# Kernel optimization log

Measured on AMD Instinct MI355X. Metric: run time of the kernel, lower is better.

The kernel has to match this reference:

```python
import jax, jax.numpy as jnp
import numpy as np

_SCAN_CHUNK = 32


def _causal_decay_scan(x, decay, init):
    """Inclusive scan out[t] = decay*out[t-1] + x[t], chunked closed form.
    x: [B,H,T,D], decay: [1,H,1], init: [B,H,D]. Returns [B,H,T,D]."""
    B, H, T, D = x.shape
    C = min(_SCAN_CHUNK, T)
    assert T % C == 0
    nC = T // C
    log_decay = jnp.log(jnp.clip(decay.astype(jnp.float32), 1e-8, None))  # [1,H,1]
    c_idx = jnp.arange(C, dtype=jnp.float32)
    log_p = log_decay[..., None] * c_idx.reshape(1, 1, C, 1)              # [1,H,C,1]
    p = jnp.exp(log_p)
    inv_p = jnp.exp(-log_p)
    init_p = jnp.exp(log_decay[..., None] * (c_idx + 1.0).reshape(1, 1, C, 1))
    # [nC, B, H, C, D] so lax.scan chains chunk states causally
    xc = x.reshape(B, H, nC, C, D).transpose(2, 0, 1, 3, 4).astype(jnp.float32)

    def step(state, chunk):  # state [B,H,D], chunk [B,H,C,D]
        cs = jnp.cumsum(chunk * inv_p, axis=2)
        out = cs * p + state[:, :, None, :] * init_p
        return out[:, :, -1, :], out

    _, outs = jax.lax.scan(step, init.astype(jnp.float32), xc)
    return outs.transpose(1, 2, 0, 3, 4).reshape(B, H, T, D).astype(x.dtype)


def _phi(x):
    return jax.nn.elu(x) + 1.0


def setup_inputs() -> dict:
    key = jax.random.key(0)
    ks = jax.random.split(key, 5)
    B, T, hidden, H = 4, 4096, 1024, 16
    s = 1.0 / np.sqrt(hidden)
    x = jax.random.normal(ks[0], (B, T, hidden), dtype=jnp.float32)
    Wqkv = jax.random.normal(ks[1], (3 * hidden, hidden), dtype=jnp.float32) * s
    Wout = jax.random.normal(ks[2], (hidden, hidden), dtype=jnp.float32) * s
    Wgate = jax.random.normal(ks[3], (hidden, hidden), dtype=jnp.float32) * s
    bgate = jnp.zeros((hidden,), dtype=jnp.float32)
    logit = float(np.log(0.95 / 0.05))  # sigmoid(logit) == 0.95
    decay_param = jnp.full((H,), logit, dtype=jnp.float32)
    return {"x": x, "Wqkv": Wqkv, "Wout": Wout, "Wgate": Wgate,
            "bgate": bgate, "decay_param": decay_param}


def reference(x, Wqkv, Wout, Wgate, bgate, decay_param):
    B, T, hidden = x.shape
    H = decay_param.shape[0]
    D = hidden // H
    qkv = x @ Wqkv.T                       # [B,T,3*hidden]
    q, k, v = jnp.split(qkv, 3, axis=-1)
    # [B,T,hidden] -> [B,H,T,D]
    q = q.reshape(B, T, H, D).transpose(0, 2, 1, 3)
    k = k.reshape(B, T, H, D).transpose(0, 2, 1, 3)
    v = v.reshape(B, T, H, D).transpose(0, 2, 1, 3)
    q = _phi(q)
    k = _phi(k)
    decay = jax.nn.sigmoid(decay_param).reshape(1, H, 1)
    kv_init = jnp.zeros((B, H, D), dtype=x.dtype)
    ksum_init = jnp.zeros((B, H, D), dtype=x.dtype)
    running_kv = _causal_decay_scan(k * v, decay, kv_init)
    running_ksum = _causal_decay_scan(k, decay, ksum_init)
    den = jnp.clip(jnp.sum(q * running_ksum, axis=-1, keepdims=True), 1e-6, None)
    out = q * running_kv / den             # [B,H,T,D]
    v_direct = v.transpose(0, 2, 1, 3).reshape(B, T, hidden)
    out = out.transpose(0, 2, 1, 3).reshape(B, T, hidden)
    g = jax.nn.sigmoid(out @ Wgate.T + bgate)
    out = g * out + (1.0 - g) * v_direct
    return out @ Wout.T
```

## Files before the change

kernel.cpp:

```cpp
#include <hip/hip_runtime.h>

typedef unsigned short u16;
typedef __bf16 bf16x8 __attribute__((ext_vector_type(8)));
typedef float f32x4 __attribute__((ext_vector_type(4)));

#define BB 4
#define TT 4096
#define HID 1024
#define NH 16
#define HD 64
#define BT (BB*TT)
#define NCH 256
#define LOG_NCH 8
#define CLEN (TT/NCH)

__device__ __forceinline__ float bf2f(u16 u) {
    return __uint_as_float(((unsigned)u) << 16);
}
__device__ __forceinline__ u16 f2bf(float f) {
    unsigned u = __float_as_uint(f);
    unsigned r = 0x7FFFu + ((u >> 16) & 1u);
    return (u16)((u + r) >> 16);
}
__device__ __forceinline__ float phi(float x) {
    return x > 0.f ? x + 1.f : __expf(x);
}
__device__ __forceinline__ float sigmoidf(float x) {
    return 1.f / (1.f + __expf(-x));
}
__device__ __forceinline__ float4 u4_to_f4(ushort4 u) {
    return make_float4(bf2f(u.x), bf2f(u.y), bf2f(u.z), bf2f(u.w));
}

#define CN1 (BT*HID/4)
#define CN2 (3*HID*HID/4)
#define CN3 (HID*HID/4)
#define CN4 (HID*HID/4)
__global__ void convert_all(const float4* __restrict__ x,    const float4* __restrict__ wqkv,
                            const float4* __restrict__ wgate, const float4* __restrict__ wout,
                            ushort4* __restrict__ xb,    ushort4* __restrict__ wqkvb,
                            ushort4* __restrict__ wgateb, ushort4* __restrict__ woutb) {
    int i = blockIdx.x * 256 + threadIdx.x;
    const float4* src; ushort4* dst; int j;
    if (i < CN1)                 { src = x;     dst = xb;     j = i; }
    else if (i < CN1+CN2)        { src = wqkv;  dst = wqkvb;  j = i - CN1; }
    else if (i < CN1+CN2+CN3)    { src = wgate; dst = wgateb; j = i - CN1 - CN2; }
    else                         { src = wout;  dst = woutb;  j = i - CN1 - CN2 - CN3; }
    float4 f = src[j];
    ushort4 u;
    u.x = f2bf(f.x); u.y = f2bf(f.y); u.z = f2bf(f.z); u.w = f2bf(f.w);
    dst[j] = u;
}

template<int EPI>
__global__ __launch_bounds__(256)
void gemm_bt(const u16* __restrict__ A, const u16* __restrict__ Bm,
             int M, int N, int K, void* __restrict__ Cout,
             const float* __restrict__ bg,
             const u16* __restrict__ attn,
             const u16* __restrict__ qkv)
{
    __shared__ u16 As[128 * 64];
    __shared__ u16 Bs[128 * 64];
    const int tid  = threadIdx.x;
    const int wave = tid >> 6;
    const int lane = tid & 63;
    const int m0 = blockIdx.y * 128;
    const int n0 = blockIdx.x * 128;
    const int mw = (wave & 1) * 64;
    const int nw = (wave >> 1) * 64;
    const int r16 = lane & 15;

    f32x4 acc[4][4];
    #pragma unroll
    for (int i = 0; i < 4; ++i)
        #pragma unroll
        for (int j = 0; j < 4; ++j)
            acc[i][j] = (f32x4){0.f, 0.f, 0.f, 0.f};

    for (int k0 = 0; k0 < K; k0 += 64) {
        #pragma unroll
        for (int i = 0; i < 4; ++i) {
            int s   = i * 4 + wave;
            int idx = s * 64 + lane;
            int pr  = idx >> 3;
            int pc  = idx & 7;
            int lc  = pc ^ (pr & 7);
            const u16* gA = A  + (size_t)(m0 + pr) * K + k0 + lc * 8;
            const u16* gB = Bm + (size_t)(n0 + pr) * K + k0 + lc * 8;
            __builtin_amdgcn_global_load_lds(
                (const __attribute__((address_space(1))) void*)gA,
                (__attribute__((address_space(3))) void*)&As[s * 512], 16, 0, 0);
            __builtin_amdgcn_global_load_lds(
                (const __attribute__((address_space(1))) void*)gB,
                (__attribute__((address_space(3))) void*)&Bs[s * 512], 16, 0, 0);
        }
        __syncthreads();
        #pragma unroll
        for (int s2 = 0; s2 < 2; ++s2) {
            const int lcq = s2 * 4 + (lane >> 4);
            const int pcq = lcq ^ (r16 & 7);
            bf16x8 af[4], bq[4];
            #pragma unroll
            for (int i = 0; i < 4; ++i)
                af[i] = *(const bf16x8*)&As[(mw + i * 16 + r16) * 64 + pcq * 8];
            #pragma unroll
            for (int j = 0; j < 4; ++j)
                bq[j] = *(const bf16x8*)&Bs[(nw + j * 16 + r16) * 64 + pcq * 8];
            #pragma unroll
            for (int i = 0; i < 4; ++i)
                #pragma unroll
                for (int j = 0; j < 4; ++j)
                    acc[i][j] = __builtin_amdgcn_mfma_f32_16x16x32_bf16(af[i], bq[j], acc[i][j], 0, 0, 0);
        }
        __syncthreads();
    }

    #pragma unroll
    for (int i = 0; i < 4; ++i) {
        int rowb = m0 + mw + i * 16 + (lane >> 4) * 4;
        #pragma unroll
        for (int j = 0; j < 4; ++j) {
            int col = n0 + nw + j * 16 + r16;
            #pragma unroll
            for (int r = 0; r < 4; ++r) {
                float v = acc[i][j][r];
                size_t row = (size_t)(rowb + r);
                if (EPI == 0) {
                    ((u16*)Cout)[row * N + col] = f2bf(v);
                } else if (EPI == 1) {
                    float g  = sigmoidf(v + bg[col]);
                    float at = bf2f(attn[row * HID + col]);
                    float vd = bf2f(qkv[row * (3 * HID) + 2 * HID + col]);
                    ((u16*)Cout)[row * HID + col] = f2bf(g * at + (1.f - g) * vd);
                } else {
                    ((float*)Cout)[row * N + col] = v;
                }
            }
        }
    }
}

__global__ void scan_finals(const u16* __restrict__ qkv, const float* __restrict__ decay_param,
                            float* __restrict__ ckv, float* __restrict__ cks) {
    int g  = blockIdx.x * 16 + (threadIdx.x >> 4);
    int sl = threadIdx.x & 15;
    int c = g & (NCH - 1);
    int h = (g >> LOG_NCH) & (NH - 1);
    int b = g >> (LOG_NCH + 4);
    float decay = sigmoidf(decay_param[h]);
    const u16* kp = qkv + (size_t)(b * TT + c * CLEN) * (3 * HID) + HID + h * HD + sl * 4;
    float4 skv = make_float4(0.f, 0.f, 0.f, 0.f);
    float4 sks = make_float4(0.f, 0.f, 0.f, 0.f);
    #pragma unroll
    for (int t = 0; t < CLEN; ++t) {
        float4 k = u4_to_f4(*(const ushort4*)kp);
        float4 v = u4_to_f4(*(const ushort4*)(kp + HID));
        k.x = phi(k.x); k.y = phi(k.y); k.z = phi(k.z); k.w = phi(k.w);
        skv.x = decay * skv.x + k.x * v.x;  skv.y = decay * skv.y + k.y * v.y;
        skv.z = decay * skv.z + k.z * v.z;  skv.w = decay * skv.w + k.w * v.w;
        sks.x = decay * sks.x + k.x;        sks.y = decay * sks.y + k.y;
        sks.z = decay * sks.z + k.z;        sks.w = decay * sks.w + k.w;
        kp += 3 * HID;
    }
    *(float4*)(ckv + (size_t)g * 64 + sl * 4) = skv;
    *(float4*)(cks + (size_t)g * 64 + sl * 4) = sks;
}

__global__ void scan_prefix(float* __restrict__ ckv, float* __restrict__ cks,
                            const float* __restrict__ decay_param) {
    int bh = blockIdx.x;
    int h  = bh & (NH - 1);
    int lane = threadIdx.x;
    float decay = sigmoidf(decay_param[h]);
    float dC = powf(decay, (float)CLEN);
    float* pkv = ckv + (size_t)bh * NCH * 64 + lane;
    float* pks = cks + (size_t)bh * NCH * 64 + lane;
    float fkv = 0.f, fks = 0.f;
    for (int c = 0; c < NCH; ++c) {
        float lkv = pkv[c * 64], lks = pks[c * 64];
        pkv[c * 64] = fkv; pks[c * 64] = fks;
        fkv = fkv * dC + lkv;
        fks = fks * dC + lks;
    }
}

__global__ void scan_apply(const u16* __restrict__ qkv, const float* __restrict__ decay_param,
                           const float* __restrict__ ckv, const float* __restrict__ cks,
                           u16* __restrict__ attn) {
    int g  = blockIdx.x * 16 + (threadIdx.x >> 4);
    int sl = threadIdx.x & 15;
    int c = g & (NCH - 1);
    int h = (g >> LOG_NCH) & (NH - 1);
    int b = g >> (LOG_NCH + 4);
    float decay = sigmoidf(decay_param[h]);
    float4 skv = *(const float4*)(ckv + (size_t)g * 64 + sl * 4);
    float4 sks = *(const float4*)(cks + (size_t)g * 64 + sl * 4);
    const u16* qp = qkv + (size_t)(b * TT + c * CLEN) * (3 * HID) + h * HD + sl * 4;
    u16* op = attn + (size_t)(b * TT + c * CLEN) * HID + h * HD + sl * 4;
    #pragma unroll
    for (int t = 0; t < CLEN; ++t) {
        float4 q = u4_to_f4(*(const ushort4*)qp);
        float4 k = u4_to_f4(*(const ushort4*)(qp + HID));
        float4 v = u4_to_f4(*(const ushort4*)(qp + 2 * HID));
        q.x = phi(q.x); q.y = phi(q.y); q.z = phi(q.z); q.w = phi(q.w);
        k.x = phi(k.x); k.y = phi(k.y); k.z = phi(k.z); k.w = phi(k.w);
        skv.x = decay * skv.x + k.x * v.x;  skv.y = decay * skv.y + k.y * v.y;
        skv.z = decay * skv.z + k.z * v.z;  skv.w = decay * skv.w + k.w * v.w;
        sks.x = decay * sks.x + k.x;        sks.y = decay * sks.y + k.y;
        sks.z = decay * sks.z + k.z;        sks.w = decay * sks.w + k.w;
        float s = q.x * sks.x + q.y * sks.y + q.z * sks.z + q.w * sks.w;
        s += __shfl_xor(s, 8);
        s += __shfl_xor(s, 4);
        s += __shfl_xor(s, 2);
        s += __shfl_xor(s, 1);
        float inv = 1.f / fmaxf(s, 1e-6f);
        ushort4 o;
        o.x = f2bf(q.x * skv.x * inv); o.y = f2bf(q.y * skv.y * inv);
        o.z = f2bf(q.z * skv.z * inv); o.w = f2bf(q.w * skv.w * inv);
        *(ushort4*)op = o;
        qp += 3 * HID;
        op += HID;
    }
}

extern "C" void kernel_launch(void* const* d_in, const int* in_sizes, int n_in,
                              void* d_out, int out_size, void* d_ws, size_t ws_size,
                              hipStream_t stream) {
    const float* x     = (const float*)d_in[0];
    const float* Wqkv  = (const float*)d_in[1];
    const float* Wout  = (const float*)d_in[2];
    const float* Wgate = (const float*)d_in[3];
    const float* bgate = (const float*)d_in[4];
    const float* decay = (const float*)d_in[5];

    u16* xb     = (u16*)d_ws;
    u16* wqkvb  = xb    + (size_t)BT * HID;
    u16* wgateb = wqkvb + (size_t)3 * HID * HID;
    u16* woutb  = wgateb + (size_t)HID * HID;
    u16* qkvb   = woutb + (size_t)HID * HID;
    u16* out2b  = qkvb  + (size_t)BT * 3 * HID;
    float* ckv  = (float*)out2b;
    float* cks  = ckv + (size_t)BB * NH * NCH * HD;
    u16* attnb  = xb;

    convert_all<<<(CN1 + CN2 + CN3 + CN4) / 256, 256, 0, stream>>>(
        (const float4*)x, (const float4*)Wqkv, (const float4*)Wgate, (const float4*)Wout,
        (ushort4*)xb, (ushort4*)wqkvb, (ushort4*)wgateb, (ushort4*)woutb);

    gemm_bt<0><<<dim3(3 * HID / 128, BT / 128), 256, 0, stream>>>(
        xb, wqkvb, BT, 3 * HID, HID, qkvb, nullptr, nullptr, nullptr);

    scan_finals<<<BB * NH * NCH / 16, 256, 0, stream>>>(qkvb, decay, ckv, cks);
    scan_prefix<<<BB * NH, 64, 0, stream>>>(ckv, cks, decay);
    scan_apply<<<BB * NH * NCH / 16, 256, 0, stream>>>(qkvb, decay, ckv, cks, attnb);

    gemm_bt<1><<<dim3(HID / 128, BT / 128), 256, 0, stream>>>(
        attnb, wgateb, BT, HID, HID, out2b, bgate, attnb, qkvb);

    gemm_bt<2><<<dim3(HID / 128, BT / 128), 256, 0, stream>>>(
        out2b, woutb, BT, HID, HID, d_out, nullptr, nullptr, nullptr);
}
```

Before: 405.3 us.

## Replace GEMM with 256x256 tile, 8-wave double-buffered software-pipelined kernel

Rewrites the bf16 GEMM used for the three projections. It now uses 256x256 block tiles with 8 waves, and each wave computes a 128x64 sub-tile. LDS is double-buffered, and async global-to-LDS loads are interleaved with register fragment reads and MFMA groups using partial vmcnt waits, barriers and s_setprio. The goal is to hide memory latency behind MFMA work and raise data reuse per loaded tile, at the cost of more registers and LDS. Fewer blocks are launched, 256 for the smaller GEMMs, which may underfill the CUs.

```diff
diff --git a/kernel.cpp b/kernel.cpp
--- a/kernel.cpp
+++ b/kernel.cpp
@@ -53,78 +53,141 @@
 }
 
 template<int EPI>
-__global__ __launch_bounds__(256)
-void gemm_bt(const u16* __restrict__ A, const u16* __restrict__ Bm,
-             int M, int N, int K, void* __restrict__ Cout,
-             const float* __restrict__ bg,
-             const u16* __restrict__ attn,
-             const u16* __restrict__ qkv)
+__global__ __launch_bounds__(512, 2)
+void gemm8p(const u16* __restrict__ A, const u16* __restrict__ Bm,
+            int M, int N, int K, void* __restrict__ Cout,
+            const float* __restrict__ bg,
+            const u16* __restrict__ attn,
+            const u16* __restrict__ qkv)
 {
-    __shared__ u16 As[128 * 64];
-    __shared__ u16 Bs[128 * 64];
+    __shared__ u16 As[2][256 * 64];
+    __shared__ u16 Bs[2][256 * 64];
     const int tid  = threadIdx.x;
     const int wave = tid >> 6;
     const int lane = tid & 63;
-    const int m0 = blockIdx.y * 128;
-    const int n0 = blockIdx.x * 128;
-    const int mw = (wave & 1) * 64;
-    const int nw = (wave >> 1) * 64;
-    const int r16 = lane & 15;
-
-    f32x4 acc[4][4];
+    const int r16  = lane & 15;
+    const int m0 = blockIdx.y * 256;
+    const int n0 = blockIdx.x * 256;
+    const int wm = (wave & 1) * 128;
+    const int wn = (wave >> 1) * 64;
+
+    const int q0 = wave * 2, q1 = wave * 2 + 1;
+    const int rsub = lane >> 3;
+    const int lcg  = (lane & 7) ^ (rsub & 7);
+    const int ldsA0 = ((q0 >> 3) * 128 + (q0 & 7) * 8) * 64;
+    const int ldsA1 = ((q1 >> 3) * 128 + (q1 & 7) * 8) * 64;
+    const int ldsB0 = ((q0 >> 2) * 64  + (q0 & 3) * 8) * 64;
+    const int ldsB1 = ((q1 >> 2) * 64  + (q1 & 3) * 8) * 64;
+    const size_t gA0 = (size_t)(m0 + (q0 >> 3) * 128 + (q0 & 7) * 8 + rsub) * K + lcg * 8;
+    const size_t gA1 = (size_t)(m0 + (q1 >> 3) * 128 + (q1 & 7) * 8 + rsub) * K + lcg * 8;
+    const size_t gB0 = (size_t)(n0 + (q0 >> 2) * 64 + (q0 & 3) * 8 + rsub) * K + lcg * 8;
+    const size_t gB1 = (size_t)(n0 + (q1 >> 2) * 64 + (q1 & 3) * 8 + rsub) * K + lcg * 8;
+    const int p0 = ((lane >> 4)      ) ^ (r16 & 7);
+    const int p1 = ((lane >> 4) + 4  ) ^ (r16 & 7);
+    const int vA0 = (wm + r16) * 64 + p0 * 8;
+    const int vA1 = (wm + r16) * 64 + p1 * 8;
+    const int vB0 = (wn + r16) * 64 + p0 * 8;
+    const int vB1 = (wn + r16) * 64 + p1 * 8;
+
+    f32x4 acc[8][4];
     #pragma unroll
-    for (int i = 0; i < 4; ++i)
+    for (int i = 0; i < 8; ++i)
         #pragma unroll
         for (int j = 0; j < 4; ++j)
             acc[i][j] = (f32x4){0.f, 0.f, 0.f, 0.f};
 
-    for (int k0 = 0; k0 < K; k0 += 64) {
+    bf16x8 afX[4][2], afY[4][2];
+    bf16x8 bqA[2][2], bqB[2][2];
+
+#define STAGE_A(K0, BUF, MQ) do {                                              \
+    __builtin_amdgcn_global_load_lds(                                          \
+        (const __attribute__((address_space(1))) void*)(A + gA0 + (size_t)((MQ)*64) * K + (K0)), \
+        (__attribute__((address_space(3))) void*)&As[BUF][ldsA0 + (MQ)*64*64], 16, 0, 0); \
+    __builtin_amdgcn_global_load_lds(                                          \
+        (const __attribute__((address_space(1))) void*)(A + gA1 + (size_t)((MQ)*64) * K + (K0)), \
+        (__attribute__((address_space(3))) void*)&As[BUF][ldsA1 + (MQ)*64*64], 16, 0, 0); \
+} while (0)
+#define STAGE_B(K0, BUF, NQ) do {                                              \
+    __builtin_amdgcn_global_load_lds(                                          \
+        (const __attribute__((address_space(1))) void*)(Bm + gB0 + (size_t)((NQ)*32) * K + (K0)), \
+        (__attribute__((address_space(3))) void*)&Bs[BUF][ldsB0 + (NQ)*32*64], 16, 0, 0); \
+    __builtin_amdgcn_global_load_lds(                                          \
+        (const __attribute__((address_space(1))) void*)(Bm + gB1 + (size_t)((NQ)*32) * K + (K0)), \
+        (__attribute__((address_space(3))) void*)&Bs[BUF][ldsB1 + (NQ)*32*64], 16, 0, 0); \
+} while (0)
+#define RDA01(BUF, MQ, DST) do {                                               \
+    DST[0][0] = *(const bf16x8*)&As[BUF][vA0 + ((MQ)*64 +  0) * 64];           \
+    DST[0][1] = *(const bf16x8*)&As[BUF][vA1 + ((MQ)*64 +  0) * 64];           \
+    DST[1][0] = *(const bf16x8*)&As[BUF][vA0 + ((MQ)*64 + 16) * 64];           \
+    DST[1][1] = *(const bf16x8*)&As[BUF][vA1 + ((MQ)*64 + 16) * 64];           \
+} while (0)
+#define RDA23(BUF, MQ, DST) do {                                               \
+    DST[2][0] = *(const bf16x8*)&As[BUF][vA0 + ((MQ)*64 + 32) * 64];           \
+    DST[2][1] = *(const bf16x8*)&As[BUF][vA1 + ((MQ)*64 + 32) * 64];           \
+    DST[3][0] = *(const bf16x8*)&As[BUF][vA0 + ((MQ)*64 + 48) * 64];           \
+    DST[3][1] = *(const bf16x8*)&As[BUF][vA1 + ((MQ)*64 + 48) * 64];           \
+} while (0)
+#define RDB(BUF, NQ, DST) do {                                                 \
+    DST[0][0] = *(const bf16x8*)&Bs[BUF][vB0 + ((NQ)*32 +  0) * 64];           \
+    DST[0][1] = *(const bf16x8*)&Bs[BUF][vB1 + ((NQ)*32 +  0) * 64];           \
+    DST[1][0] = *(const bf16x8*)&Bs[BUF][vB0 + ((NQ)*32 + 16) * 64];           \
+    DST[1][1] = *(const bf16x8*)&Bs[BUF][vB1 + ((NQ)*32 + 16) * 64];           \
+} while (0)
+#define MFMAQ(MQ, NQ, AF, BQ) do {                                             \
+    __builtin_amdgcn_s_setprio(1);                                             \
+    _Pragma("unroll") for (int i_ = 0; i_ < 4; ++i_)                           \
+    _Pragma("unroll") for (int j_ = 0; j_ < 2; ++j_)                           \
+    _Pragma("unroll") for (int k_ = 0; k_ < 2; ++k_)                           \
+        acc[(MQ)*4 + i_][(NQ)*2 + j_] = __builtin_amdgcn_mfma_f32_16x16x32_bf16( \
+            AF[i_][k_], BQ[j_][k_], acc[(MQ)*4 + i_][(NQ)*2 + j_], 0, 0, 0);   \
+    __builtin_amdgcn_s_setprio(0);                                             \
+} while (0)
+#define VMBAR(NV) do {                                                         \
+    asm volatile("s_waitcnt vmcnt(" #NV ")" ::: "memory");                     \
+    __builtin_amdgcn_s_barrier();                                              \
+    asm volatile("" ::: "memory");                                             \
+} while (0)
+
+    const int niter = K >> 7;
+
+    STAGE_A(0, 0, 0); STAGE_B(0, 0, 0); STAGE_A(0, 0, 1); STAGE_B(0, 0, 1);
+    STAGE_A(64, 1, 0); STAGE_B(64, 1, 0);
+    VMBAR(4);
+    RDA01(0, 0, afX); RDA23(0, 0, afX); RDB(0, 0, bqA);
+
+    for (int i = 0; i < niter - 1; ++i) {
+        const int kb = i * 128;
+        STAGE_A(kb +  64, 1, 1); RDB(0, 1, bqB); RDA01(0, 1, afY); MFMAQ(0, 0, afX, bqA);
+        STAGE_B(kb +  64, 1, 1); RDA23(0, 1, afY);                 MFMAQ(0, 1, afX, bqB); VMBAR(4);
+        STAGE_A(kb + 128, 0, 0); RDA01(1, 0, afX);                 MFMAQ(1, 0, afY, bqA);
+        STAGE_B(kb + 128, 0, 0); RDA23(1, 0, afX); RDB(1, 0, bqA); MFMAQ(1, 1, afY, bqB); VMBAR(4);
+        STAGE_A(kb + 128, 0, 1); RDB(1, 1, bqB); RDA01(1, 1, afY); MFMAQ(0, 0, afX, bqA);
+        STAGE_B(kb + 128, 0, 1); RDA23(1, 1, afY);                 MFMAQ(0, 1, afX, bqB); VMBAR(4);
+        STAGE_A(kb + 192, 1, 0); RDA01(0, 0, afX);                 MFMAQ(1, 0, afY, bqA);
+        STAGE_B(kb + 192, 1, 0); RDA23(0, 0, afX); RDB(0, 0, bqA); MFMAQ(1, 1, afY, bqB); VMBAR(4);
+    }
+
+    {
+        const int kb = (niter - 1) * 128;
+        STAGE_A(kb + 64, 1, 1); RDB(0, 1, bqB); RDA01(0, 1, afY);  MFMAQ(0, 0, afX, bqA);
+        STAGE_B(kb + 64, 1, 1); RDA23(0, 1, afY);                  MFMAQ(0, 1, afX, bqB); VMBAR(4);
+        RDA01(1, 0, afX);                                          MFMAQ(1, 0, afY, bqA);
+        RDA23(1, 0, afX); RDB(1, 0, bqA);                          MFMAQ(1, 1, afY, bqB); VMBAR(0);
+        RDB(1, 1, bqB); RDA01(1, 1, afY);                          MFMAQ(0, 0, afX, bqA);
+        RDA23(1, 1, afY);                                          MFMAQ(0, 1, afX, bqB);
+        MFMAQ(1, 0, afY, bqA);
+        MFMAQ(1, 1, afY, bqB);
+    }
+
+    #pragma unroll
+    for (int mi = 0; mi < 8; ++mi) {
+        int rowb = m0 + wm + mi * 16 + (lane >> 4) * 4;
         #pragma unroll
-        for (int i = 0; i < 4; ++i) {
-            int s   = i * 4 + wave;
-            int idx = s * 64 + lane;
-            int pr  = idx >> 3;
-            int pc  = idx & 7;
-            int lc  = pc ^ (pr & 7);
-            const u16* gA = A  + (size_t)(m0 + pr) * K + k0 + lc * 8;
-            const u16* gB = Bm + (size_t)(n0 + pr) * K + k0 + lc * 8;
-            __builtin_amdgcn_global_load_lds(
-                (const __attribute__((address_space(1))) void*)gA,
-                (__attribute__((address_space(3))) void*)&As[s * 512], 16, 0, 0);
-            __builtin_amdgcn_global_load_lds(
-                (const __attribute__((address_space(1))) void*)gB,
-                (__attribute__((address_space(3))) void*)&Bs[s * 512], 16, 0, 0);
-        }
-        __syncthreads();
-        #pragma unroll
-        for (int s2 = 0; s2 < 2; ++s2) {
-            const int lcq = s2 * 4 + (lane >> 4);
-            const int pcq = lcq ^ (r16 & 7);
-            bf16x8 af[4], bq[4];
-            #pragma unroll
-            for (int i = 0; i < 4; ++i)
-                af[i] = *(const bf16x8*)&As[(mw + i * 16 + r16) * 64 + pcq * 8];
-            #pragma unroll
-            for (int j = 0; j < 4; ++j)
-                bq[j] = *(const bf16x8*)&Bs[(nw + j * 16 + r16) * 64 + pcq * 8];
-            #pragma unroll
-            for (int i = 0; i < 4; ++i)
-                #pragma unroll
-                for (int j = 0; j < 4; ++j)
-                    acc[i][j] = __builtin_amdgcn_mfma_f32_16x16x32_bf16(af[i], bq[j], acc[i][j], 0, 0, 0);
-        }
-        __syncthreads();
-    }
-
-    #pragma unroll
-    for (int i = 0; i < 4; ++i) {
-        int rowb = m0 + mw + i * 16 + (lane >> 4) * 4;
-        #pragma unroll
-        for (int j = 0; j < 4; ++j) {
-            int col = n0 + nw + j * 16 + r16;
+        for (int nj = 0; nj < 4; ++nj) {
+            int col = n0 + wn + nj * 16 + r16;
             #pragma unroll
             for (int r = 0; r < 4; ++r) {
-                float v = acc[i][j][r];
+                float v = acc[mi][nj][r];
                 size_t row = (size_t)(rowb + r);
                 if (EPI == 0) {
                     ((u16*)Cout)[row * N + col] = f2bf(v);
@@ -139,6 +202,13 @@
             }
         }
     }
+#undef STAGE_A
+#undef STAGE_B
+#undef RDA01
+#undef RDA23
+#undef RDB
+#undef MFMAQ
+#undef VMBAR
 }
 
 __global__ void scan_finals(const u16* __restrict__ qkv, const float* __restrict__ decay_param,
@@ -248,16 +318,16 @@
         (const float4*)x, (const float4*)Wqkv, (const float4*)Wgate, (const float4*)Wout,
         (ushort4*)xb, (ushort4*)wqkvb, (ushort4*)wgateb, (ushort4*)woutb);
 
-    gemm_bt<0><<<dim3(3 * HID / 128, BT / 128), 256, 0, stream>>>(
+    gemm8p<0><<<dim3(3 * HID / 256, BT / 256), 512, 0, stream>>>(
         xb, wqkvb, BT, 3 * HID, HID, qkvb, nullptr, nullptr, nullptr);
 
     scan_finals<<<BB * NH * NCH / 16, 256, 0, stream>>>(qkvb, decay, ckv, cks);
     scan_prefix<<<BB * NH, 64, 0, stream>>>(ckv, cks, decay);
     scan_apply<<<BB * NH * NCH / 16, 256, 0, stream>>>(qkvb, decay, ckv, cks, attnb);
 
-    gemm_bt<1><<<dim3(HID / 128, BT / 128), 256, 0, stream>>>(
+    gemm8p<1><<<dim3(HID / 256, BT / 256), 512, 0, stream>>>(
         attnb, wgateb, BT, HID, HID, out2b, bgate, attnb, qkvb);
 
-    gemm_bt<2><<<dim3(HID / 128, BT / 128), 256, 0, stream>>>(
+    gemm8p<2><<<dim3(HID / 256, BT / 256), 512, 0, stream>>>(
         out2b, woutb, BT, HID, HID, d_out, nullptr, nullptr, nullptr);
 }
```

Result: slower. 490.4 us (+21.0%).
